# Kernel tuning notes

Measured on AMD Instinct MI355X. Metric: run time of the kernel, lower is better.

The kernel has to match this reference:

```python
import jax, jax.numpy as jnp
import numpy as np

N_NODES = 50000
N_EDGES = 640000
IN_DIM = 4
EMBED = 128
OUT_DIM = 1
N_LAYERS = 3


def setup_inputs() -> dict:
    key = jax.random.key(0)
    ks = jax.random.split(key, 12)
    node_feats = jax.random.normal(ks[0], (N_NODES, IN_DIM), dtype=jnp.float32)
    src = jax.random.randint(ks[1], (N_EDGES,), 0, N_NODES, dtype=jnp.int64 if jax.config.x64_enabled else jnp.int32)
    dst = jax.random.randint(ks[2], (N_EDGES,), 0, N_NODES, dtype=jnp.int64 if jax.config.x64_enabled else jnp.int32)
    s = 1.0 / np.sqrt(EMBED)
    W_emb = jax.random.normal(ks[3], (IN_DIM, EMBED), dtype=jnp.float32) * (1.0 / np.sqrt(IN_DIM))
    b_emb = jnp.zeros((EMBED,), dtype=jnp.float32)
    W_g = jax.random.normal(ks[4], (N_LAYERS, EMBED, EMBED), dtype=jnp.float32) * s
    b_g = jnp.zeros((N_LAYERS, EMBED), dtype=jnp.float32)
    W_o1 = jax.random.normal(ks[5], (EMBED, EMBED), dtype=jnp.float32) * s
    b_o1 = jnp.zeros((EMBED,), dtype=jnp.float32)
    W_o2 = jax.random.normal(ks[6], (EMBED, OUT_DIM), dtype=jnp.float32) * s
    b_o2 = jnp.zeros((OUT_DIM,), dtype=jnp.float32)
    return {"node_feats": node_feats, "src": src, "dst": dst,
            "W_emb": W_emb, "b_emb": b_emb, "W_g": W_g, "b_g": b_g,
            "W_o1": W_o1, "b_o1": b_o1, "W_o2": W_o2, "b_o2": b_o2}


def reference(node_feats, src, dst, W_emb, b_emb, W_g, b_g, W_o1, b_o1, W_o2, b_o2):
    n = node_feats.shape[0]
    ones = jnp.ones(src.shape[0], dtype=node_feats.dtype)
    # DGL GraphConv norm='both': symmetric degree normalization, degrees clamped to >=1
    out_deg = jnp.clip(jax.ops.segment_sum(ones, src, num_segments=n), 1.0)
    in_deg = jnp.clip(jax.ops.segment_sum(ones, dst, num_segments=n), 1.0)
    norm_src = (out_deg ** -0.5)[:, None]  # [N,1]
    norm_dst = (in_deg ** -0.5)[:, None]   # [N,1]

    h = node_feats @ W_emb + b_emb  # [N, E]
    for l in range(W_g.shape[0]):
        x = h * norm_src                                        # scale sources
        agg = jax.ops.segment_sum(x[src], dst, num_segments=n)  # SpMM gather/scatter
        h = agg * norm_dst
        h = h @ W_g[l] + b_g[l]
        h = jax.nn.relu(h)
    h = jax.nn.relu(h @ W_o1 + b_o1)
    return h @ W_o2 + b_o2  # [N, out_dim]
```

## Files before the change

kernel.cpp:

```cpp
#include <hip/hip_runtime.h>

#define NN 50000
#define NE 640000
#define SCAN_B 196

typedef short bf16x8 __attribute__((ext_vector_type(8)));
typedef float f32x4 __attribute__((ext_vector_type(4)));

__device__ __forceinline__ unsigned short f2bf(float f) {
  unsigned int u = __float_as_uint(f);
  unsigned int r = (u + 0x7FFFu + ((u >> 16) & 1u)) >> 16;
  return (unsigned short)r;
}
__device__ __forceinline__ float bf2f(unsigned short h) {
  return __uint_as_float(((unsigned int)h) << 16);
}

typedef const __attribute__((address_space(1))) void* gptr_t;
typedef __attribute__((address_space(3))) void* lptr_t;
__device__ __forceinline__ void gload16(const void* g, void* l) {
  __builtin_amdgcn_global_load_lds((gptr_t)g, (lptr_t)l, 16, 0, 0);
}

__global__ __launch_bounds__(256) void k_deg(const int* __restrict__ src,
                                             const int* __restrict__ dst,
                                             int* __restrict__ out_cnt,
                                             int* __restrict__ in_cnt,
                                             int* __restrict__ rank) {
  int e = blockIdx.x * 256 + threadIdx.x;
  if (e < NE) {
    atomicAdd(&out_cnt[src[e]], 1);
    rank[e] = atomicAdd(&in_cnt[dst[e]], 1);
  }
}

__global__ __launch_bounds__(256) void k_scan1(const int* __restrict__ out_cnt,
                                               const int* __restrict__ in_cnt,
                                               float* __restrict__ nsrc,
                                               float* __restrict__ ndst,
                                               int* __restrict__ bsum) {
  int t = threadIdx.x, i = blockIdx.x * 256 + t;
  int v = 0;
  if (i < NN) {
    v = in_cnt[i];
    nsrc[i] = 1.0f / sqrtf((float)max(out_cnt[i], 1));
    ndst[i] = 1.0f / sqrtf((float)max(v, 1));
  }
  int s = v;
#pragma unroll
  for (int o = 32; o >= 1; o >>= 1) s += __shfl_down(s, o);
  __shared__ int ws4[4];
  if ((t & 63) == 0) ws4[t >> 6] = s;
  __syncthreads();
  if (t == 0) bsum[blockIdx.x] = ws4[0] + ws4[1] + ws4[2] + ws4[3];
}

__global__ __launch_bounds__(256) void k_scan2(const int* __restrict__ bsum,
                                               int* __restrict__ boff) {
  int t = threadIdx.x, lane = t & 63, w = t >> 6;
  int v = (t < SCAN_B) ? bsum[t] : 0;
  int sc = v;
#pragma unroll
  for (int o = 1; o < 64; o <<= 1) {
    int x = __shfl_up(sc, o);
    if (lane >= o) sc += x;
  }
  __shared__ int wtot[4];
  if (lane == 63) wtot[w] = sc;
  __syncthreads();
  int base = 0;
  for (int i = 0; i < w; ++i) base += wtot[i];
  if (t < SCAN_B) boff[t] = base + sc - v;
}

__global__ __launch_bounds__(256) void k_scan3(const int* __restrict__ cnt,
                                               const int* __restrict__ boff,
                                               int* __restrict__ row_start) {
  int b = blockIdx.x, t = threadIdx.x, lane = t & 63, w = t >> 6;
  int i = b * 256 + t;
  int v = (i < NN) ? cnt[i] : 0;
  int sc = v;
#pragma unroll
  for (int o = 1; o < 64; o <<= 1) {
    int x = __shfl_up(sc, o);
    if (lane >= o) sc += x;
  }
  __shared__ int wtot[4];
  if (lane == 63) wtot[w] = sc;
  __syncthreads();
  int base = boff[b];
  for (int j = 0; j < w; ++j) base += wtot[j];
  if (i < NN) row_start[i] = base + sc - v;
}

__global__ __launch_bounds__(256) void k_fill(const int* __restrict__ src,
                                              const int* __restrict__ dst,
                                              const int* __restrict__ row_start,
                                              const int* __restrict__ rank,
                                              int* __restrict__ col) {
  int e = blockIdx.x * 256 + threadIdx.x;
  if (e < NE) {
    int d = dst[e];
    col[row_start[d] + rank[e]] = src[e];
  }
}

__global__ __launch_bounds__(256) void k_prep(const float* __restrict__ Wg,
                                              const float* __restrict__ Wo1,
                                              unsigned short* __restrict__ wt) {
  int idx = blockIdx.x * 256 + threadIdx.x;
  int mat = idx >> 14, rem = idx & 16383;
  int k = rem >> 7, n = rem & 127;
  const float* Wsrc = (mat < 3) ? (Wg + mat * 16384) : Wo1;
  float v = Wsrc[k * 128 + n];
  unsigned short hi = f2bf(v);
  float lo = v - bf2f(hi);
  unsigned short* base = wt + mat * 32768;
  base[n * 128 + k] = hi;
  base[16384 + n * 128 + k] = f2bf(lo);
}

__global__ __launch_bounds__(256) void k_embed(const float* __restrict__ nf,
                                               const float* __restrict__ W,
                                               const float* __restrict__ b,
                                               const float* __restrict__ nsrc,
                                               float* __restrict__ xs) {
  int idx = blockIdx.x * 256 + threadIdx.x;
  int n = idx >> 7, j = idx & 127;
  const float* f = nf + n * 4;
  float acc = b[j];
  acc += f[0] * W[j] + f[1] * W[128 + j] + f[2] * W[256 + j] + f[3] * W[384 + j];
  xs[idx] = acc * nsrc[n];
}

__global__ __launch_bounds__(256) void k_spmm(const float* __restrict__ xs,
                                              unsigned short* __restrict__ ahi,
                                              unsigned short* __restrict__ alo,
                                              const int* __restrict__ col,
                                              const int* __restrict__ row_start,
                                              const int* __restrict__ in_cnt,
                                              const float* __restrict__ ndst) {
  int node = blockIdx.x * 4 + (threadIdx.x >> 6);
  int lane = threadIdx.x & 63;
  int half = lane >> 5;
  int ql = lane & 31;
  int start = row_start[node];
  int cnt = in_cnt[node];
  float4 acc = make_float4(0.f, 0.f, 0.f, 0.f);
  const float4* X4 = (const float4*)xs;
  for (int base = 0; base < cnt; base += 64) {
    int m = min(cnt - base, 64);
    int ccol = (lane < m) ? col[start + base + lane] : 0;
    for (int jj = 0; jj < m; jj += 8) {
      int i0 = jj + half, i1 = i0 + 2, i2 = i0 + 4, i3 = i0 + 6;
      int mm = m - 1;
      int s0 = __shfl(ccol, min(i0, mm));
      int s1 = __shfl(ccol, min(i1, mm));
      int s2 = __shfl(ccol, min(i2, mm));
      int s3 = __shfl(ccol, min(i3, mm));
      float f0 = (i0 < m) ? 1.f : 0.f;
      float f1 = (i1 < m) ? 1.f : 0.f;
      float f2 = (i2 < m) ? 1.f : 0.f;
      float f3 = (i3 < m) ? 1.f : 0.f;
      float4 v0 = X4[(size_t)s0 * 32 + ql];
      float4 v1 = X4[(size_t)s1 * 32 + ql];
      float4 v2 = X4[(size_t)s2 * 32 + ql];
      float4 v3 = X4[(size_t)s3 * 32 + ql];
      acc.x = fmaf(f0, v0.x, acc.x); acc.y = fmaf(f0, v0.y, acc.y);
      acc.z = fmaf(f0, v0.z, acc.z); acc.w = fmaf(f0, v0.w, acc.w);
      acc.x = fmaf(f1, v1.x, acc.x); acc.y = fmaf(f1, v1.y, acc.y);
      acc.z = fmaf(f1, v1.z, acc.z); acc.w = fmaf(f1, v1.w, acc.w);
      acc.x = fmaf(f2, v2.x, acc.x); acc.y = fmaf(f2, v2.y, acc.y);
      acc.z = fmaf(f2, v2.z, acc.z); acc.w = fmaf(f2, v2.w, acc.w);
      acc.x = fmaf(f3, v3.x, acc.x); acc.y = fmaf(f3, v3.y, acc.y);
      acc.z = fmaf(f3, v3.z, acc.z); acc.w = fmaf(f3, v3.w, acc.w);
    }
  }
  acc.x += __shfl_down(acc.x, 32);
  acc.y += __shfl_down(acc.y, 32);
  acc.z += __shfl_down(acc.z, 32);
  acc.w += __shfl_down(acc.w, 32);
  if (half == 0) {
    float nd = ndst[node];
    float v0 = acc.x * nd, v1 = acc.y * nd, v2 = acc.z * nd, v3 = acc.w * nd;
    ushort4 h, l;
    h.x = f2bf(v0); l.x = f2bf(v0 - bf2f(h.x));
    h.y = f2bf(v1); l.y = f2bf(v1 - bf2f(h.y));
    h.z = f2bf(v2); l.z = f2bf(v2 - bf2f(h.z));
    h.w = f2bf(v3); l.w = f2bf(v3 - bf2f(h.w));
    *(ushort4*)(ahi + (size_t)node * 128 + ql * 4) = h;
    *(ushort4*)(alo + (size_t)node * 128 + ql * 4) = l;
  }
}

__global__ __launch_bounds__(256) void k_gemm_mfma(
    const unsigned short* __restrict__ Ahi, const unsigned short* __restrict__ Alo,
    const unsigned short* __restrict__ Wth, const unsigned short* __restrict__ Wtl,
    const float* __restrict__ bias, float* __restrict__ outf,
    unsigned short* __restrict__ outhi, unsigned short* __restrict__ outlo,
    const float* __restrict__ nsrc, const float* __restrict__ W_o2,
    const float* __restrict__ b_o2, int M, int mode) {
  __shared__ unsigned short sm[2 * 64 * 128];
  __shared__ float smred[4][64];
  int tid = threadIdx.x;
  int lane = tid & 63, w = tid >> 6;
  int tile0 = blockIdx.x * 64;

  {
    int slot = lane & 15;
#pragma unroll
    for (int j = 0; j < 4; ++j) {
      int ldsoff = w * 4096 + j * 1024;
      int row = (ldsoff >> 8) + (lane >> 4);
      int grow = tile0 + row;
      if (grow > M - 1) grow = M - 1;
      size_t gsrc = (size_t)grow * 256 + (size_t)(((slot ^ (row & 7)) << 4));
      gload16((const char*)Ahi + gsrc, (char*)sm + ldsoff);
      gload16((const char*)Alo + gsrc, (char*)sm + 16384 + ldsoff);
    }
  }

  bf16x8 bh[2][4], bl[2][4];
  {
    int koff = (lane >> 4) * 8;
#pragma unroll
    for (int cf = 0; cf < 2; ++cf) {
      int n = w * 32 + cf * 16 + (lane & 15);
      const unsigned short* ph = Wth + (size_t)n * 128 + koff;
      const unsigned short* pl = Wtl + (size_t)n * 128 + koff;
#pragma unroll
      for (int kc = 0; kc < 4; ++kc) {
        bh[cf][kc] = *(const bf16x8*)(ph + kc * 32);
        bl[cf][kc] = *(const bf16x8*)(pl + kc * 32);
      }
    }
  }

  f32x4 acc[4][2] = {};
  __syncthreads();

  int r15 = lane & 15, kq = lane >> 4;
  for (int kc = 0; kc < 4; ++kc) {
    bf16x8 ah[4], al[4];
#pragma unroll
    for (int m = 0; m < 4; ++m) {
      int row = m * 16 + r15;
      int boff = row * 256 + ((((kc * 4 + kq) ^ (row & 7))) << 4);
      ah[m] = *(const bf16x8*)((const char*)sm + boff);
      al[m] = *(const bf16x8*)((const char*)sm + 16384 + boff);
    }
#pragma unroll
    for (int m = 0; m < 4; ++m)
#pragma unroll
      for (int cf = 0; cf < 2; ++cf) {
        acc[m][cf] = __builtin_amdgcn_mfma_f32_16x16x32_bf16(ah[m], bh[cf][kc], acc[m][cf], 0, 0, 0);
        acc[m][cf] = __builtin_amdgcn_mfma_f32_16x16x32_bf16(ah[m], bl[cf][kc], acc[m][cf], 0, 0, 0);
        acc[m][cf] = __builtin_amdgcn_mfma_f32_16x16x32_bf16(al[m], bh[cf][kc], acc[m][cf], 0, 0, 0);
      }
  }

  if (mode == 3) {
    float w2v[2], bv2[2];
#pragma unroll
    for (int cf = 0; cf < 2; ++cf) {
      int colg = w * 32 + cf * 16 + r15;
      w2v[cf] = W_o2[colg];
      bv2[cf] = bias[colg];
    }
#pragma unroll
    for (int m = 0; m < 4; ++m) {
#pragma unroll
      for (int i = 0; i < 4; ++i) {
        float p = fmaxf(acc[m][0][i] + bv2[0], 0.f) * w2v[0] +
                  fmaxf(acc[m][1][i] + bv2[1], 0.f) * w2v[1];
#pragma unroll
        for (int msk = 1; msk < 16; msk <<= 1) p += __shfl_xor(p, msk);
        if (r15 == 0) smred[w][m * 16 + kq * 4 + i] = p;
      }
    }
    __syncthreads();
    if (tid < 64) {
      int gr = tile0 + tid;
      if (gr < M)
        outf[gr] = smred[0][tid] + smred[1][tid] + smred[2][tid] + smred[3][tid] + b_o2[0];
    }
    return;
  }
#pragma unroll
  for (int cf = 0; cf < 2; ++cf) {
    int colg = w * 32 + cf * 16 + r15;
    float bv = bias[colg];
#pragma unroll
    for (int m = 0; m < 4; ++m) {
#pragma unroll
      for (int i = 0; i < 4; ++i) {
        int gr = tile0 + m * 16 + kq * 4 + i;
        if (gr < M) {
          float v = fmaxf(acc[m][cf][i] + bv, 0.f);
          if (mode == 0) {
            outf[(size_t)gr * 128 + colg] = v * nsrc[gr];
          } else {
            unsigned short h = f2bf(v);
            outhi[(size_t)gr * 128 + colg] = h;
            outlo[(size_t)gr * 128 + colg] = f2bf(v - bf2f(h));
          }
        }
      }
    }
  }
}

extern "C" void kernel_launch(void* const* d_in, const int* in_sizes, int n_in,
                              void* d_out, int out_size, void* d_ws, size_t ws_size,
                              hipStream_t stream) {
  const float* node_feats = (const float*)d_in[0];
  const int* src = (const int*)d_in[1];
  const int* dst = (const int*)d_in[2];
  const float* W_emb = (const float*)d_in[3];
  const float* b_emb = (const float*)d_in[4];
  const float* W_g = (const float*)d_in[5];
  const float* b_g = (const float*)d_in[6];
  const float* W_o1 = (const float*)d_in[7];
  const float* b_o1 = (const float*)d_in[8];
  const float* W_o2 = (const float*)d_in[9];
  const float* b_o2 = (const float*)d_in[10];
  float* out = (float*)d_out;

  char* ws = (char*)d_ws;
  int* out_cnt   = (int*)(ws + 0);
  int* in_cnt    = (int*)(ws + 200704);
  int* row_start = (int*)(ws + 401408);
  float* nsrc    = (float*)(ws + 602112);
  float* ndst    = (float*)(ws + 802816);
  int* bsum      = (int*)(ws + 1003520);
  int* boff      = (int*)(ws + 1004544);
  int* col       = (int*)(ws + 1005568);
  unsigned short* wt = (unsigned short*)(ws + 3565568);
  float* X       = (float*)(ws + 3827712);
  unsigned short* Xu = (unsigned short*)(ws + 3827712);
  int* rank      = (int*)(ws + 3827712);
  unsigned short* Ahi = (unsigned short*)(ws + 29427712);
  unsigned short* Alo = (unsigned short*)(ws + 42227712);

  hipMemsetAsync(d_ws, 0, 401408, stream);

  k_deg<<<(NE + 255) / 256, 256, 0, stream>>>(src, dst, out_cnt, in_cnt, rank);
  k_scan1<<<SCAN_B, 256, 0, stream>>>(out_cnt, in_cnt, nsrc, ndst, bsum);
  k_scan2<<<1, 256, 0, stream>>>(bsum, boff);
  k_scan3<<<SCAN_B, 256, 0, stream>>>(in_cnt, boff, row_start);
  k_fill<<<(NE + 255) / 256, 256, 0, stream>>>(src, dst, row_start, rank, col);
  k_prep<<<256, 256, 0, stream>>>(W_g, W_o1, wt);
  k_embed<<<(NN * 128) / 256, 256, 0, stream>>>(node_feats, W_emb, b_emb, nsrc, X);

  int gemm_grid = (NN + 63) / 64;
  for (int l = 0; l < 3; ++l) {
    k_spmm<<<NN / 4, 256, 0, stream>>>(X, Ahi, Alo, col, row_start, in_cnt, ndst);
    unsigned short* wth = wt + l * 32768;
    unsigned short* wtl = wth + 16384;
    if (l < 2) {
      k_gemm_mfma<<<gemm_grid, 256, 0, stream>>>(Ahi, Alo, wth, wtl, b_g + l * 128,
                                                 X, nullptr, nullptr, nsrc,
                                                 nullptr, nullptr, NN, 0);
    } else {
      k_gemm_mfma<<<gemm_grid, 256, 0, stream>>>(Ahi, Alo, wth, wtl, b_g + l * 128,
                                                 nullptr, Xu, Xu + 6400000, nsrc,
                                                 nullptr, nullptr, NN, 1);
    }
  }
  k_gemm_mfma<<<gemm_grid, 256, 0, stream>>>(Xu, Xu + 6400000, wt + 3 * 32768,
                                             wt + 3 * 32768 + 16384, b_o1,
                                             out, nullptr, nullptr, nsrc,
                                             W_o2, b_o2, NN, 3);
}
```

Before: 385.3 us.

## Replicate degree counters eight ways and fuse scan and prep kernels

Degree-counting atomics now go to eight replicated count arrays, chosen by block index, so fewer threads contend on the same address. The scan step merges the replicas and records per-replica offsets that the fill step uses to place edges. The separate block-offset scan kernel is removed: each scan3 block recomputes its base from the block sums. The embed and weight-prep kernels are merged into one launch. The cost is a larger memset, more memory traffic in scan1 and an extra gather in fill.

```diff
diff --git a/kernel.cpp b/kernel.cpp
--- a/kernel.cpp
+++ b/kernel.cpp
@@ -2,6 +2,7 @@
 
 #define NN 50000
 #define NE 640000
+#define NPAD 50176
 #define SCAN_B 196
 
 typedef short bf16x8 __attribute__((ext_vector_type(8)));
@@ -24,29 +25,42 @@
 
 __global__ __launch_bounds__(256) void k_deg(const int* __restrict__ src,
                                              const int* __restrict__ dst,
-                                             int* __restrict__ out_cnt,
-                                             int* __restrict__ in_cnt,
+                                             int* __restrict__ rep_out,
+                                             int* __restrict__ rep_in,
                                              int* __restrict__ rank) {
   int e = blockIdx.x * 256 + threadIdx.x;
+  int r = blockIdx.x & 7;
   if (e < NE) {
-    atomicAdd(&out_cnt[src[e]], 1);
-    rank[e] = atomicAdd(&in_cnt[dst[e]], 1);
-  }
-}
-
-__global__ __launch_bounds__(256) void k_scan1(const int* __restrict__ out_cnt,
-                                               const int* __restrict__ in_cnt,
+    atomicAdd(&rep_out[r * NPAD + src[e]], 1);
+    rank[e] = atomicAdd(&rep_in[r * NPAD + dst[e]], 1);
+  }
+}
+
+__global__ __launch_bounds__(256) void k_scan1(const int* __restrict__ rep_out,
+                                               const int* __restrict__ rep_in,
                                                float* __restrict__ nsrc,
                                                float* __restrict__ ndst,
+                                               int* __restrict__ in_cnt,
+                                               int* __restrict__ repoff,
                                                int* __restrict__ bsum) {
-  int t = threadIdx.x, i = blockIdx.x * 256 + t;
-  int v = 0;
-  if (i < NN) {
-    v = in_cnt[i];
-    nsrc[i] = 1.0f / sqrtf((float)max(out_cnt[i], 1));
-    ndst[i] = 1.0f / sqrtf((float)max(v, 1));
-  }
-  int s = v;
+  int t = threadIdx.x, n = blockIdx.x * 256 + t;
+  int tot_in = 0;
+  if (n < NN) {
+    int od = 0;
+#pragma unroll
+    for (int r = 0; r < 8; ++r) od += rep_out[r * NPAD + n];
+    int pf = 0;
+#pragma unroll
+    for (int r = 0; r < 8; ++r) {
+      repoff[n * 8 + r] = pf;
+      pf += rep_in[r * NPAD + n];
+    }
+    tot_in = pf;
+    in_cnt[n] = tot_in;
+    nsrc[n] = 1.0f / sqrtf((float)max(od, 1));
+    ndst[n] = 1.0f / sqrtf((float)max(tot_in, 1));
+  }
+  int s = tot_in;
 #pragma unroll
   for (int o = 32; o >= 1; o >>= 1) s += __shfl_down(s, o);
   __shared__ int ws4[4];
@@ -55,40 +69,32 @@
   if (t == 0) bsum[blockIdx.x] = ws4[0] + ws4[1] + ws4[2] + ws4[3];
 }
 
-__global__ __launch_bounds__(256) void k_scan2(const int* __restrict__ bsum,
-                                               int* __restrict__ boff) {
-  int t = threadIdx.x, lane = t & 63, w = t >> 6;
-  int v = (t < SCAN_B) ? bsum[t] : 0;
+__global__ __launch_bounds__(256) void k_scan3(const int* __restrict__ in_cnt,
+                                               const int* __restrict__ bsum,
+                                               int* __restrict__ row_start) {
+  int b = blockIdx.x, t = threadIdx.x, lane = t & 63, w = t >> 6;
+  __shared__ int wtot[4];
+  __shared__ int sbase;
+  {
+    int v = (t < b) ? bsum[t] : 0;
+#pragma unroll
+    for (int o = 32; o >= 1; o >>= 1) v += __shfl_down(v, o);
+    if (lane == 0) wtot[w] = v;
+    __syncthreads();
+    if (t == 0) sbase = wtot[0] + wtot[1] + wtot[2] + wtot[3];
+    __syncthreads();
+  }
+  int i = b * 256 + t;
+  int v = (i < NN) ? in_cnt[i] : 0;
   int sc = v;
 #pragma unroll
   for (int o = 1; o < 64; o <<= 1) {
     int x = __shfl_up(sc, o);
     if (lane >= o) sc += x;
   }
-  __shared__ int wtot[4];
   if (lane == 63) wtot[w] = sc;
   __syncthreads();
-  int base = 0;
-  for (int i = 0; i < w; ++i) base += wtot[i];
-  if (t < SCAN_B) boff[t] = base + sc - v;
-}
-
-__global__ __launch_bounds__(256) void k_scan3(const int* __restrict__ cnt,
-                                               const int* __restrict__ boff,
-                                               int* __restrict__ row_start) {
-  int b = blockIdx.x, t = threadIdx.x, lane = t & 63, w = t >> 6;
-  int i = b * 256 + t;
-  int v = (i < NN) ? cnt[i] : 0;
-  int sc = v;
-#pragma unroll
-  for (int o = 1; o < 64; o <<= 1) {
-    int x = __shfl_up(sc, o);
-    if (lane >= o) sc += x;
-  }
-  __shared__ int wtot[4];
-  if (lane == 63) wtot[w] = sc;
-  __syncthreads();
-  int base = boff[b];
+  int base = sbase;
   for (int j = 0; j < w; ++j) base += wtot[j];
   if (i < NN) row_start[i] = base + sc - v;
 }
@@ -96,41 +102,45 @@
 __global__ __launch_bounds__(256) void k_fill(const int* __restrict__ src,
                                               const int* __restrict__ dst,
                                               const int* __restrict__ row_start,
+                                              const int* __restrict__ repoff,
                                               const int* __restrict__ rank,
                                               int* __restrict__ col) {
   int e = blockIdx.x * 256 + threadIdx.x;
+  int r = blockIdx.x & 7;
   if (e < NE) {
     int d = dst[e];
-    col[row_start[d] + rank[e]] = src[e];
-  }
-}
-
-__global__ __launch_bounds__(256) void k_prep(const float* __restrict__ Wg,
-                                              const float* __restrict__ Wo1,
-                                              unsigned short* __restrict__ wt) {
-  int idx = blockIdx.x * 256 + threadIdx.x;
-  int mat = idx >> 14, rem = idx & 16383;
-  int k = rem >> 7, n = rem & 127;
-  const float* Wsrc = (mat < 3) ? (Wg + mat * 16384) : Wo1;
-  float v = Wsrc[k * 128 + n];
-  unsigned short hi = f2bf(v);
-  float lo = v - bf2f(hi);
-  unsigned short* base = wt + mat * 32768;
-  base[n * 128 + k] = hi;
-  base[16384 + n * 128 + k] = f2bf(lo);
-}
-
-__global__ __launch_bounds__(256) void k_embed(const float* __restrict__ nf,
-                                               const float* __restrict__ W,
-                                               const float* __restrict__ b,
-                                               const float* __restrict__ nsrc,
-                                               float* __restrict__ xs) {
-  int idx = blockIdx.x * 256 + threadIdx.x;
-  int n = idx >> 7, j = idx & 127;
-  const float* f = nf + n * 4;
-  float acc = b[j];
-  acc += f[0] * W[j] + f[1] * W[128 + j] + f[2] * W[256 + j] + f[3] * W[384 + j];
-  xs[idx] = acc * nsrc[n];
+    col[row_start[d] + repoff[d * 8 + r] + rank[e]] = src[e];
+  }
+}
+
+__global__ __launch_bounds__(256) void k_embed_prep(const float* __restrict__ nf,
+                                                    const float* __restrict__ W,
+                                                    const float* __restrict__ b,
+                                                    const float* __restrict__ nsrc,
+                                                    float* __restrict__ xs,
+                                                    const float* __restrict__ Wg,
+                                                    const float* __restrict__ Wo1,
+                                                    unsigned short* __restrict__ wt) {
+  int bid = blockIdx.x;
+  if (bid < 25000) {
+    int idx = bid * 256 + threadIdx.x;
+    int n = idx >> 7, j = idx & 127;
+    const float* f = nf + n * 4;
+    float acc = b[j];
+    acc += f[0] * W[j] + f[1] * W[128 + j] + f[2] * W[256 + j] + f[3] * W[384 + j];
+    xs[idx] = acc * nsrc[n];
+  } else {
+    int idx = (bid - 25000) * 256 + threadIdx.x;
+    int mat = idx >> 14, rem = idx & 16383;
+    int k = rem >> 7, n = rem & 127;
+    const float* Wsrc = (mat < 3) ? (Wg + mat * 16384) : Wo1;
+    float v = Wsrc[k * 128 + n];
+    unsigned short hi = f2bf(v);
+    float lo = v - bf2f(hi);
+    unsigned short* base = wt + mat * 32768;
+    base[n * 128 + k] = hi;
+    base[16384 + n * 128 + k] = f2bf(lo);
+  }
 }
 
 __global__ __launch_bounds__(256) void k_spmm(const float* __restrict__ xs,
@@ -327,30 +337,30 @@
   float* out = (float*)d_out;
 
   char* ws = (char*)d_ws;
-  int* out_cnt   = (int*)(ws + 0);
-  int* in_cnt    = (int*)(ws + 200704);
-  int* row_start = (int*)(ws + 401408);
-  float* nsrc    = (float*)(ws + 602112);
-  float* ndst    = (float*)(ws + 802816);
-  int* bsum      = (int*)(ws + 1003520);
-  int* boff      = (int*)(ws + 1004544);
-  int* col       = (int*)(ws + 1005568);
-  unsigned short* wt = (unsigned short*)(ws + 3565568);
-  float* X       = (float*)(ws + 3827712);
-  unsigned short* Xu = (unsigned short*)(ws + 3827712);
-  int* rank      = (int*)(ws + 3827712);
-  unsigned short* Ahi = (unsigned short*)(ws + 29427712);
-  unsigned short* Alo = (unsigned short*)(ws + 42227712);
-
-  hipMemsetAsync(d_ws, 0, 401408, stream);
-
-  k_deg<<<(NE + 255) / 256, 256, 0, stream>>>(src, dst, out_cnt, in_cnt, rank);
-  k_scan1<<<SCAN_B, 256, 0, stream>>>(out_cnt, in_cnt, nsrc, ndst, bsum);
-  k_scan2<<<1, 256, 0, stream>>>(bsum, boff);
-  k_scan3<<<SCAN_B, 256, 0, stream>>>(in_cnt, boff, row_start);
-  k_fill<<<(NE + 255) / 256, 256, 0, stream>>>(src, dst, row_start, rank, col);
-  k_prep<<<256, 256, 0, stream>>>(W_g, W_o1, wt);
-  k_embed<<<(NN * 128) / 256, 256, 0, stream>>>(node_feats, W_emb, b_emb, nsrc, X);
+  int* rep_out   = (int*)(ws + 0);
+  int* rep_in    = (int*)(ws + 1605632);
+  int* in_cnt    = (int*)(ws + 3211264);
+  int* row_start = (int*)(ws + 3411968);
+  float* nsrc    = (float*)(ws + 3612672);
+  float* ndst    = (float*)(ws + 3813376);
+  int* repoff    = (int*)(ws + 4014080);
+  int* bsum      = (int*)(ws + 5619712);
+  int* col       = (int*)(ws + 5620736);
+  unsigned short* wt = (unsigned short*)(ws + 8180736);
+  float* X       = (float*)(ws + 8442880);
+  unsigned short* Xu = (unsigned short*)(ws + 8442880);
+  int* rank      = (int*)(ws + 8442880);
+  unsigned short* Ahi = (unsigned short*)(ws + 34042880);
+  unsigned short* Alo = (unsigned short*)(ws + 46842880);
+
+  hipMemsetAsync(d_ws, 0, 3211264, stream);
+
+  k_deg<<<(NE + 255) / 256, 256, 0, stream>>>(src, dst, rep_out, rep_in, rank);
+  k_scan1<<<SCAN_B, 256, 0, stream>>>(rep_out, rep_in, nsrc, ndst, in_cnt, repoff, bsum);
+  k_scan3<<<SCAN_B, 256, 0, stream>>>(in_cnt, bsum, row_start);
+  k_fill<<<(NE + 255) / 256, 256, 0, stream>>>(src, dst, row_start, repoff, rank, col);
+  k_embed_prep<<<25256, 256, 0, stream>>>(node_feats, W_emb, b_emb, nsrc, X,
+                                          W_g, W_o1, wt);
 
   int gemm_grid = (NN + 63) / 64;
   for (int l = 0; l < 3; ++l) {
```

New measurement: 390.1 us. Within noise of the previous version (+1.2%).
